# Kernel optimization log

Hardware: AMD Instinct MI355X
Metric: run time of the kernel (lower is better)

## Reference

```python
import jax, jax.numpy as jnp
import numpy as np

PC_RANGE = np.array([-40.0, -40.0, -1.0, 40.0, 40.0, 5.4], np.float32)
RADIUS = 39.0
STEP_SIZE = 0.5
WORLD_LEN = 200
NUM_CLASSES = 17
FAST_THRES = 1e-7
W_ENT = 0.01
W_DIST = 0.01
W_SEM = 1.0
ALPHA_INIT = 1e-6

_xyz_min_w = PC_RANGE[:3]
_xyz_max_w = PC_RANGE[3:]
_rng = _xyz_max_w - _xyz_min_w
BG_LEN = float((np.floor_divide(_rng[0], 2.0) - RADIUS) / RADIUS)
SCENE_CENTER = ((_xyz_min_w + _xyz_max_w) * 0.5).astype(np.float32)
_Z = float(_rng[2] / _rng[0])
XYZ_MIN = np.array([-1.0 - BG_LEN, -1.0 - BG_LEN, -_Z], np.float32)
XYZ_MAX = np.array([1.0 + BG_LEN, 1.0 + BG_LEN, _Z], np.float32)
ACT_SHIFT = float(np.log(1.0 / (1.0 - ALPHA_INIT) - 1.0))
DIST_THRES = (2.0 + 2.0 * BG_LEN) / WORLD_LEN * STEP_SIZE * 0.95

N_INNER = int(2.0 / (2.0 + 2.0 * BG_LEN) * WORLD_LEN / STEP_SIZE) + 1
N_OUTER = N_INNER // 15
_b_in = np.linspace(0.0, 2.0, N_INNER + 1)
_b_out = 2.0 / np.linspace(1.0, 1.0 / 64.0, N_OUTER + 1)
T_VALS = np.concatenate([(_b_in[1:] + _b_in[:-1]) * 0.5, (_b_out[1:] + _b_out[:-1]) * 0.5]).astype(np.float32)

_freq = np.array([1163161, 2309034, 188743, 2997643, 20317180, 852476, 243808, 2457947, 497017, 2731022, 7224789, 214411435, 5565043, 63191967, 76098082, 128860031, 141625221], np.float64)
CLASS_W = (1.0 / np.log(_freq + 0.001)).astype(np.float32)


def trilinear(vol, g):
    # vol: [X,Y,Z,C]; g: [P,3] fractional voxel indices (align_corners=True, zeros padding)
    sizes = jnp.array(vol.shape[:3])
    g0f = jnp.floor(g)
    frac = g - g0f
    g0 = g0f.astype(jnp.int32)
    out = jnp.zeros((g.shape[0], vol.shape[3]), vol.dtype)
    for dx in (0, 1):
        for dy in (0, 1):
            for dz in (0, 1):
                off = jnp.array([dx, dy, dz])
                idx = g0 + off
                w = jnp.prod(jnp.where(off == 1, frac, 1.0 - frac), axis=-1)
                valid = jnp.all((idx >= 0) & (idx < sizes), axis=-1)
                ic = jnp.clip(idx, 0, sizes - 1)
                v = vol[ic[:, 0], ic[:, 1], ic[:, 2]]
                out = out + (w * valid)[:, None] * v
    return out


def _render_losses(density_b, semantic_b, rays_b, bda_b):
    t = jnp.asarray(T_VALS)  # [S]
    gt_depth = rays_b[:, 2]
    gt_depth = jnp.where(gt_depth > 52.0, 0.0, gt_depth)
    ray_valid = gt_depth > 0.0  # [N]
    gt_sem = rays_b[:, 3].astype(jnp.int32)
    ro = rays_b[:, 4:7]
    rd = rays_b[:, 7:10]
    rays_o = (ro - SCENE_CENTER) / RADIUS
    rays_d = rd / jnp.linalg.norm(rd, axis=-1, keepdims=True)
    pts = rays_o[:, None, :] + rays_d[:, None, :] * t[None, :, None]  # [N,S,3]
    nrm = jnp.linalg.norm(pts, axis=-1, keepdims=True)
    inner = (nrm <= 1.0)[..., 0]
    pts = jnp.where(nrm <= 1.0, pts, pts / nrm * (1.0 + BG_LEN - BG_LEN / nrm))
    pts = jnp.einsum('ij,nsj->nsi', bda_b, pts)
    # cumdist_thres: sequential cumulative-distance scan per ray (keep outer points spaced > thres)
    dist = jnp.linalg.norm(pts[:, 1:] - pts[:, :-1], axis=-1)  # [N,S-1]
    def step(cum, d):
        cum = cum + d
        over = cum > DIST_THRES
        return jnp.where(over, 0.0, cum), over
    _, over = jax.lax.scan(step, jnp.zeros(pts.shape[0], pts.dtype), dist.T)
    keep = jnp.concatenate([inner[:, :1], inner[:, 1:] | over.T], axis=1)
    # trilinear grid sample (align_corners=True)
    g = (pts - XYZ_MIN) / (XYZ_MAX - XYZ_MIN)
    gi = (g * (jnp.array([200.0, 200.0, 16.0]) - 1.0)).reshape(-1, 3)
    dens = trilinear(density_b[..., None], gi)[:, 0].reshape(pts.shape[:2])  # [N,S]
    sem = trilinear(semantic_b, gi).reshape(pts.shape[0], pts.shape[1], NUM_CLASSES)  # [N,S,C]
    # Raw2Alpha with interval=0.5: alpha = 1 - (1+exp(d+shift))^(-interval)
    alpha = 1.0 - jnp.power(1.0 + jnp.exp(dens + ACT_SHIFT), -0.5)
    alpha = jnp.where(keep & ray_valid[:, None], alpha, 0.0)
    alpha = jnp.where(alpha > FAST_THRES, alpha, 0.0)  # fast_color_thres cull
    # Alphas2Weights: per-ray exclusive transmittance cumprod
    om = 1.0 - alpha
    Tinc = jnp.cumprod(om, axis=1)
    Texcl = jnp.concatenate([jnp.ones_like(Tinc[:, :1]), Tinc[:, :-1]], axis=1)
    weights = alpha * Texcl
    alphainv_last = Tinc[:, -1]
    pk = weights > FAST_THRES
    w = jnp.where(pk, weights, 0.0)
    # segment_coo semantic render (segment-sum over step dim)
    sem_r = jnp.einsum('ns,nsc->nc', w, sem)
    logp = jax.nn.log_softmax(sem_r, axis=-1)
    nll = -jnp.take_along_axis(logp, gt_sem[:, None], axis=1)[:, 0]
    cw = jnp.asarray(CLASS_W)
    wy = cw[gt_sem] * ray_valid.astype(cw.dtype)
    loss_sem = jnp.sum(wy * nll) / jnp.maximum(jnp.sum(wy), 1e-12)
    # entropy of last transmittance over valid rays
    p = jnp.clip(alphainv_last, 1e-6, 1.0 - 1e-6)
    ent = -(p * jnp.log(p) + (1.0 - p) * jnp.log(1.0 - p))
    nv = jnp.maximum(jnp.sum(ray_valid), 1)
    loss_ent = jnp.sum(jnp.where(ray_valid, ent, 0.0)) / nv
    # flatten_eff_distloss with interval = 1/n_max
    s = 1.0 - 1.0 / (1.0 + t)
    m = jnp.broadcast_to(s[None, :], w.shape)
    n_max = jnp.maximum(jnp.sum(pk), 1)
    interval = 1.0 / n_max
    wm = w * m
    wp = jnp.cumsum(w, axis=1) - w
    wmp = jnp.cumsum(wm, axis=1) - wm
    loss_bi = 2.0 * w * (m * wp - wmp)
    loss_uni = (1.0 / 3.0) * interval * w * w
    loss_dist = (jnp.sum(loss_bi) + jnp.sum(loss_uni)) / nv
    return W_SEM * loss_sem, W_ENT * loss_ent, W_DIST * loss_dist


def setup_inputs():
    key = jax.random.key(0)
    ks = jax.random.split(key, 6)
    B, N = 1, 8192
    density = jax.random.normal(ks[0], (B, 200, 200, 16), jnp.float32)
    semantic = jax.random.normal(ks[1], (B, 200, 200, 16, 17), jnp.float32)
    depth = jax.random.uniform(ks[2], (B, N), jnp.float32, 0.1, 60.0)
    sem_lbl = jax.random.randint(ks[3], (B, N), 0, 17).astype(jnp.float32)
    ro = jax.random.normal(ks[4], (B, N, 3), jnp.float32) + jnp.array([0.0, 0.0, 1.5])
    rd = jax.random.normal(ks[5], (B, N, 3), jnp.float32)
    rd = rd / jnp.linalg.norm(rd, axis=-1, keepdims=True)
    rays = jnp.concatenate([jnp.zeros((B, N, 2)), depth[..., None], sem_lbl[..., None], ro, rd], axis=-1)
    bda = jnp.broadcast_to(jnp.eye(3, dtype=jnp.float32), (B, 3, 3))
    return {"density": density, "semantic": semantic, "rays": rays, "bda": bda}


def reference(density, semantic, rays, bda):
    B = density.shape[0]
    ls, le, ld = 0.0, 0.0, 0.0
    for b in range(B):
        a, c, d = _render_losses(density[b], semantic[b], rays[b], bda[b])
        ls, le, ld = ls + a, le + c, ld + d
    return (ls / B, le / B, ld / B)
```

## Files before the change

### kernel.cpp

```cpp
#include <hip/hip_runtime.h>
#include <math.h>


#define DXX 200
#define DYY 200
#define DZZ 16
#define NC 17
#define S_TOT 416
#define N_IN 390
#define CHUNKS 7
#define RPB 4

typedef float v4u __attribute__((ext_vector_type(4), aligned(4), may_alias));

__constant__ double c_freq[NC] = {1163161.0, 2309034.0, 188743.0, 2997643.0,
  20317180.0, 852476.0, 243808.0, 2457947.0, 497017.0, 2731022.0, 7224789.0,
  214411435.0, 5565043.0, 63191967.0, 76098082.0, 128860031.0, 141625221.0};

__device__ __forceinline__ float iscan_add(float x, int lane) {
#pragma unroll
  for (int off = 1; off < 64; off <<= 1) {
    float y = __shfl_up(x, off);
    if (lane >= off) x += y;
  }
  return x;
}
__device__ __forceinline__ float iscan_mul(float x, int lane) {
#pragma unroll
  for (int off = 1; off < 64; off <<= 1) {
    float y = __shfl_up(x, off);
    if (lane >= off) x *= y;
  }
  return x;
}

__global__ __launch_bounds__(256) void nerf_zero(float* acc) {
  if (threadIdx.x < 16) acc[threadIdx.x] = 0.f;
}

__global__ __launch_bounds__(256) void nerf_main(
    const float* __restrict__ density,
    const float* __restrict__ semantic,
    const float* __restrict__ rays,
    const float* __restrict__ bda,
    float* __restrict__ acc_g,
    int nrays) {
  __shared__ float s_t[CHUNKS * 64];
  __shared__ float s_dist[RPB][S_TOT];
  __shared__ unsigned long long s_keep[RPB][CHUNKS];
  __shared__ float s_acc[8];

  const int lane = threadIdx.x & 63;
  const int wv = threadIdx.x >> 6;
  const int ray = blockIdx.x * RPB + wv;

  const double BG = (double)(1.0f / 39.0f);
  const float BGf = (float)BG;
  const float DTH = (float)((2.0 + 2.0 * BG) / 200.0 * 0.5 * 0.95);
  const float xminf = (float)(-1.0 - BG);
  const float xmaxf = (float)(1.0 + BG);
  const float zf = 6.4f / 80.0f;
  const float sxy = 199.0f / (xmaxf - xminf);
  const float szc = 15.0f / (zf + zf);
  const float ACTS = -13.815509557964274f;

  if (threadIdx.x < 8) s_acc[threadIdx.x] = 0.f;

  for (int i = threadIdx.x; i < CHUNKS * 64; i += 256) {
    double td;
    if (i < N_IN) {
      td = (2.0 * i + 1.0) / 390.0;
    } else {
      int j = i - N_IN;
      const double stp = (1.0 / 64.0 - 1.0) / 26.0;
      double l0 = 1.0 + j * stp;
      double l1 = (j + 1 >= 26) ? (1.0 / 64.0) : (1.0 + (j + 1) * stp);
      td = 1.0 / l0 + 1.0 / l1;
    }
    s_t[i] = (float)td;
  }
  __syncthreads();

  bool doit = false;
  float rox = 0, roy = 0, roz = 0, rdx = 0, rdy = 0, rdz = 0;
  float b00 = 0, b01 = 0, b02 = 0, b10 = 0, b11 = 0, b12 = 0, b20 = 0, b21 = 0, b22 = 0;
  int ysem = 0;
  if (ray < nrays) {
    const float* rp = rays + (size_t)ray * 10;
    float dep = rp[2];
    doit = (dep > 0.f) && (dep <= 52.f);
    ysem = (int)rp[3];
    ysem = ysem < 0 ? 0 : (ysem > NC - 1 ? NC - 1 : ysem);
    const float czc = (-1.0f + 5.4f) * 0.5f;
    rox = rp[4] / 39.0f;
    roy = rp[5] / 39.0f;
    roz = (rp[6] - czc) / 39.0f;
    float d0 = rp[7], d1 = rp[8], d2 = rp[9];
    float rn = sqrtf(d0 * d0 + d1 * d1 + d2 * d2);
    rdx = d0 / rn; rdy = d1 / rn; rdz = d2 / rn;
    b00 = bda[0]; b01 = bda[1]; b02 = bda[2];
    b10 = bda[3]; b11 = bda[4]; b12 = bda[5];
    b20 = bda[6]; b21 = bda[7]; b22 = bda[8];
  }

  auto compute_pt = [&](int s, float& tx, float& ty, float& tz, float& tt,
                        bool& inner) {
    tt = s_t[s];
    float qx = rox + rdx * tt;
    float qy = roy + rdy * tt;
    float qz = roz + rdz * tt;
    float nr = sqrtf(qx * qx + qy * qy + qz * qz);
    inner = (nr <= 1.0f) && (s < S_TOT);
    if (nr > 1.0f) {
      float sc = (1.0f + BGf - BGf / nr) / nr;
      qx *= sc; qy *= sc; qz *= sc;
    }
    tx = b00 * qx + b01 * qy + b02 * qz;
    ty = b10 * qx + b11 * qy + b12 * qz;
    tz = b20 * qx + b21 * qy + b22 * qz;
  };

  if (doit) {
    for (int c = 0; c < CHUNKS; c++) {
      int s = c * 64 + lane;
      float tx, ty, tz, tt; bool inner;
      compute_pt(s, tx, ty, tz, tt, inner);
      unsigned long long bal = __ballot(inner);
      if (lane == 0) s_keep[wv][c] = bal;
      float nx = __shfl(tx, lane + 1);
      float ny = __shfl(ty, lane + 1);
      float nz = __shfl(tz, lane + 1);
      if (c < CHUNKS - 1) {
        float hx, hy, hz, ht; bool hi;
        compute_pt((c + 1) * 64, hx, hy, hz, ht, hi);
        if (lane == 63) { nx = hx; ny = hy; nz = hz; }
      }
      if (s < S_TOT - 1) {
        float ex = nx - tx, ey = ny - ty, ez = nz - tz;
        s_dist[wv][s] = sqrtf(ex * ex + ey * ey + ez * ez);
      }
    }
  }
  __syncthreads();

  if (doit && lane == 0) {
    float cum = 0.f;
    for (int c = 0; c < CHUNKS; c++) {
      unsigned long long k = s_keep[wv][c];
      int b0 = (c == 0) ? 1 : 0;
      for (int b = b0; b < 64; b++) {
        int s = c * 64 + b;
        if (s >= S_TOT) break;
        cum += s_dist[wv][s - 1];
        if (cum > DTH) { cum = 0.f; k |= (1ull << b); }
      }
      s_keep[wv][c] = k;
    }
  }
  __syncthreads();

  float out_sem[NC];
  if (doit) {
#pragma unroll
    for (int j = 0; j < NC; j++) out_sem[j] = 0.f;
    float carry = 1.f, carryW = 0.f, carryWM = 0.f;
    float sum_bi = 0.f, sum_w2 = 0.f, pkcf = 0.f;

    for (int c = 0; c < CHUNKS; c++) {
      int s = c * 64 + lane;
      float tx, ty, tz, tt; bool inner;
      compute_pt(s, tx, ty, tz, tt, inner);
      float m_ = 1.0f - 1.0f / (1.0f + tt);
      bool keep = (s_keep[wv][c] >> lane) & 1ull;

      int ix = 0, iy = 0, iz = 0;
      float fx = 0.f, fy = 0.f, fz = 0.f;
      float a = 0.f;
      if (keep) {
        float gx = (tx - xminf) * sxy;
        float gy = (ty - xminf) * sxy;
        float gz = (tz + zf) * szc;
        float hx = floorf(gx), hy = floorf(gy), hz = floorf(gz);
        ix = (int)hx; iy = (int)hy; iz = (int)hz;
        fx = gx - hx; fy = gy - hy; fz = gz - hz;
        float wx0 = 1.f - fx, wy0 = 1.f - fy, wz0 = 1.f - fz;
        bool vx0 = (unsigned)ix < (unsigned)DXX, vx1 = (unsigned)(ix + 1) < (unsigned)DXX;
        bool vy0 = (unsigned)iy < (unsigned)DYY, vy1 = (unsigned)(iy + 1) < (unsigned)DYY;
        bool vz0 = (unsigned)iz < (unsigned)DZZ, vz1 = (unsigned)(iz + 1) < (unsigned)DZZ;
        float dens = 0.f;
        if (vx0 && vy0 && vz0) dens += wx0 * wy0 * wz0 * density[((size_t)ix * DYY + iy) * DZZ + iz];
        if (vx0 && vy0 && vz1) dens += wx0 * wy0 * fz  * density[((size_t)ix * DYY + iy) * DZZ + iz + 1];
        if (vx0 && vy1 && vz0) dens += wx0 * fy  * wz0 * density[((size_t)ix * DYY + (iy + 1)) * DZZ + iz];
        if (vx0 && vy1 && vz1) dens += wx0 * fy  * fz  * density[((size_t)ix * DYY + (iy + 1)) * DZZ + iz + 1];
        if (vx1 && vy0 && vz0) dens += fx  * wy0 * wz0 * density[((size_t)(ix + 1) * DYY + iy) * DZZ + iz];
        if (vx1 && vy0 && vz1) dens += fx  * wy0 * fz  * density[((size_t)(ix + 1) * DYY + iy) * DZZ + iz + 1];
        if (vx1 && vy1 && vz0) dens += fx  * fy  * wz0 * density[((size_t)(ix + 1) * DYY + (iy + 1)) * DZZ + iz];
        if (vx1 && vy1 && vz1) dens += fx  * fy  * fz  * density[((size_t)(ix + 1) * DYY + (iy + 1)) * DZZ + iz + 1];
        float u = expf(dens + ACTS);
        a = -expm1f(-0.5f * log1pf(u));
        if (!(a > 1e-7f)) a = 0.f;
      }

      float om = 1.f - a;
      float ip = iscan_mul(om, lane);
      float ex = __shfl_up(ip, 1); if (lane == 0) ex = 1.f;
      float wgt = a * carry * ex;
      carry *= __shfl(ip, 63);
      float w = (wgt > 1e-7f) ? wgt : 0.f;
      if (w > 0.f) pkcf += 1.f;

      float wm = w * m_;
      float isw = iscan_add(w, lane);
      float iswm = iscan_add(wm, lane);
      float exw = __shfl_up(isw, 1);  if (lane == 0) exw = 0.f;
      float exwm = __shfl_up(iswm, 1); if (lane == 0) exwm = 0.f;
      sum_bi += 2.f * w * (m_ * (carryW + exw) - (carryWM + exwm));
      sum_w2 += w * w;
      carryW += __shfl(isw, 63);
      carryWM += __shfl(iswm, 63);

      if (w > 0.f) {
        float wx0 = 1.f - fx, wy0 = 1.f - fy, wz0 = 1.f - fz;
        bool vx0 = (unsigned)ix < (unsigned)DXX, vx1 = (unsigned)(ix + 1) < (unsigned)DXX;
        bool vy0 = (unsigned)iy < (unsigned)DYY, vy1 = (unsigned)(iy + 1) < (unsigned)DYY;
        bool vz0 = (unsigned)iz < (unsigned)DZZ, vz1 = (unsigned)(iz + 1) < (unsigned)DZZ;
#define SEM_CORNER(V, WX, WY, WZ, XI, YI, ZI)                                      \
        if (V) {                                                                    \
          float wc = w * (WX) * (WY) * (WZ);                                        \
          const float* sp = semantic + (((size_t)(XI) * DYY + (YI)) * DZZ + (ZI)) * NC; \
          const v4u* sp4 = (const v4u*)sp;                                          \
          v4u q0 = sp4[0], q1 = sp4[1], q2 = sp4[2], q3 = sp4[3];                   \
          float qs = sp[16];                                                        \
          out_sem[0]  += wc * q0[0];  out_sem[1]  += wc * q0[1];                    \
          out_sem[2]  += wc * q0[2];  out_sem[3]  += wc * q0[3];                    \
          out_sem[4]  += wc * q1[0];  out_sem[5]  += wc * q1[1];                    \
          out_sem[6]  += wc * q1[2];  out_sem[7]  += wc * q1[3];                    \
          out_sem[8]  += wc * q2[0];  out_sem[9]  += wc * q2[1];                    \
          out_sem[10] += wc * q2[2];  out_sem[11] += wc * q2[3];                    \
          out_sem[12] += wc * q3[0];  out_sem[13] += wc * q3[1];                    \
          out_sem[14] += wc * q3[2];  out_sem[15] += wc * q3[3];                    \
          out_sem[16] += wc * qs;                                                   \
        }
        SEM_CORNER(vx0 && vy0 && vz0, wx0, wy0, wz0, ix, iy, iz)
        SEM_CORNER(vx0 && vy0 && vz1, wx0, wy0, fz,  ix, iy, iz + 1)
        SEM_CORNER(vx0 && vy1 && vz0, wx0, fy,  wz0, ix, iy + 1, iz)
        SEM_CORNER(vx0 && vy1 && vz1, wx0, fy,  fz,  ix, iy + 1, iz + 1)
        SEM_CORNER(vx1 && vy0 && vz0, fx,  wy0, wz0, ix + 1, iy, iz)
        SEM_CORNER(vx1 && vy0 && vz1, fx,  wy0, fz,  ix + 1, iy, iz + 1)
        SEM_CORNER(vx1 && vy1 && vz0, fx,  fy,  wz0, ix + 1, iy + 1, iz)
        SEM_CORNER(vx1 && vy1 && vz1, fx,  fy,  fz,  ix + 1, iy + 1, iz + 1)
#undef SEM_CORNER
      }
    }

    float r0 = sum_bi, r1 = sum_w2, r2 = pkcf;
#pragma unroll
    for (int off = 32; off >= 1; off >>= 1) {
      r0 += __shfl_xor(r0, off);
      r1 += __shfl_xor(r1, off);
      r2 += __shfl_xor(r2, off);
#pragma unroll
      for (int j = 0; j < NC; j++) out_sem[j] += __shfl_xor(out_sem[j], off);
    }
    if (lane == 0) {
      float M = out_sem[0];
#pragma unroll
      for (int j = 1; j < NC; j++) M = fmaxf(M, out_sem[j]);
      float se = 0.f;
#pragma unroll
      for (int j = 0; j < NC; j++) se += expf(out_sem[j] - M);
      float lse = M + logf(se);
      float sy = 0.f;
#pragma unroll
      for (int j = 0; j < NC; j++) if (j == ysem) sy = out_sem[j];
      float nll = lse - sy;
      float cw = (float)(1.0 / log(c_freq[ysem] + 0.001));
      float p = fminf(fmaxf(carry, 1e-6f), 1.0f - 1e-6f);
      float ent = -(p * logf(p) + (1.f - p) * logf(1.f - p));
      atomicAdd(&s_acc[0], cw * nll);
      atomicAdd(&s_acc[1], cw);
      atomicAdd(&s_acc[2], ent);
      atomicAdd(&s_acc[3], 1.f);
      atomicAdd(&s_acc[4], r0);
      atomicAdd(&s_acc[5], r1);
      atomicAdd(&s_acc[6], r2);
    }
  }

  __syncthreads();
  if (threadIdx.x == 0 && s_acc[3] > 0.f) {
#pragma unroll
    for (int i = 0; i < 7; i++) atomicAdd(&acc_g[i], s_acc[i]);
  }
}

__global__ __launch_bounds__(64) void nerf_fin(const float* __restrict__ acc,
                                               float* __restrict__ out) {
  if (threadIdx.x == 0) {
    float ls = acc[0] / fmaxf(acc[1], 1e-12f);
    float nv = fmaxf(acc[3], 1.f);
    float le = acc[2] / nv;
    float nmax = fmaxf(acc[6], 1.f);
    float ld = (acc[4] + (1.f / 3.f) * (1.f / nmax) * acc[5]) / nv;
    out[0] = 1.0f * ls;
    out[1] = 0.01f * le;
    out[2] = 0.01f * ld;
  }
}

extern "C" void kernel_launch(void* const* d_in, const int* in_sizes, int n_in,
                              void* d_out, int out_size, void* d_ws, size_t ws_size,
                              hipStream_t stream) {
  const float* density = (const float*)d_in[0];
  const float* semantic = (const float*)d_in[1];
  const float* rays = (const float*)d_in[2];
  const float* bda = (const float*)d_in[3];
  float* out = (float*)d_out;
  float* acc = (float*)d_ws;
  int nrays = in_sizes[2] / 10;
  nerf_zero<<<1, 256, 0, stream>>>(acc);
  int nb = (nrays + RPB - 1) / RPB;
  nerf_main<<<nb, 64 * RPB, 0, stream>>>(density, semantic, rays, bda, acc, nrays);
  nerf_fin<<<1, 64, 0, stream>>>(acc, out);
}
```

Baseline: 305.3 us.

## Use persistent waves with atomic ray queue and fuse sample passes

Replaces one-ray-per-wave launch with a capped persistent grid in which each wave pulls rays from an atomic counter, skipping invalid rays immediately. Merges the density sampling into the first pass, skipping gathers for chunks whose z is fully out of the grid, and keeps alpha in registers. Replaces the serial distance filter with a bitmask and ffs walk that only visits short segments. Adds vector loads for fully interior corners. It relies on the counter in the workspace being zeroed and on wave-local LDS ordering replacing block barriers, and it costs more registers.

```diff
diff --git a/kernel.cpp b/kernel.cpp
--- a/kernel.cpp
+++ b/kernel.cpp
@@ -10,8 +10,10 @@
 #define N_IN 390
 #define CHUNKS 7
 #define RPB 4
+#define NBLOCKS 1280
 
 typedef float v4u __attribute__((ext_vector_type(4), aligned(4), may_alias));
+typedef float v2u __attribute__((ext_vector_type(2), aligned(4), may_alias));
 
 __constant__ double c_freq[NC] = {1163161.0, 2309034.0, 188743.0, 2997643.0,
   20317180.0, 852476.0, 243808.0, 2457947.0, 497017.0, 2731022.0, 7224789.0,
@@ -38,7 +40,7 @@
   if (threadIdx.x < 16) acc[threadIdx.x] = 0.f;
 }
 
-__global__ __launch_bounds__(256) void nerf_main(
+__global__ __launch_bounds__(256, 5) void nerf_main(
     const float* __restrict__ density,
     const float* __restrict__ semantic,
     const float* __restrict__ rays,
@@ -48,19 +50,18 @@
   __shared__ float s_t[CHUNKS * 64];
   __shared__ float s_dist[RPB][S_TOT];
   __shared__ unsigned long long s_keep[RPB][CHUNKS];
+  __shared__ unsigned long long s_big[RPB][CHUNKS];
   __shared__ float s_acc[8];
 
   const int lane = threadIdx.x & 63;
   const int wv = threadIdx.x >> 6;
-  const int ray = blockIdx.x * RPB + wv;
 
   const double BG = (double)(1.0f / 39.0f);
   const float BGf = (float)BG;
   const float DTH = (float)((2.0 + 2.0 * BG) / 200.0 * 0.5 * 0.95);
   const float xminf = (float)(-1.0 - BG);
-  const float xmaxf = (float)(1.0 + BG);
   const float zf = 6.4f / 80.0f;
-  const float sxy = 199.0f / (xmaxf - xminf);
+  const float sxy = 199.0f / ((float)(1.0 + BG) - xminf);
   const float szc = 15.0f / (zf + zf);
   const float ACTS = -13.815509557964274f;
 
@@ -81,52 +82,59 @@
   }
   __syncthreads();
 
-  bool doit = false;
-  float rox = 0, roy = 0, roz = 0, rdx = 0, rdy = 0, rdz = 0;
-  float b00 = 0, b01 = 0, b02 = 0, b10 = 0, b11 = 0, b12 = 0, b20 = 0, b21 = 0, b22 = 0;
-  int ysem = 0;
-  if (ray < nrays) {
+  const float A0 = -expm1f(-0.5f * log1pf(expf(ACTS)));
+
+  const float b00 = bda[0], b01 = bda[1], b02 = bda[2];
+  const float b10 = bda[3], b11 = bda[4], b12 = bda[5];
+  const float b20 = bda[6], b21 = bda[7], b22 = bda[8];
+
+  int* cnt = (int*)(acc_g + 8);
+
+  for (;;) {
+    int ray;
+    if (lane == 0) ray = atomicAdd(cnt, 1);
+    ray = __shfl(ray, 0);
+    if (ray >= nrays) break;
+
     const float* rp = rays + (size_t)ray * 10;
     float dep = rp[2];
-    doit = (dep > 0.f) && (dep <= 52.f);
-    ysem = (int)rp[3];
+    bool doit = (dep > 0.f) && (dep <= 52.f);
+    if (!doit) continue;
+    int ysem = (int)rp[3];
     ysem = ysem < 0 ? 0 : (ysem > NC - 1 ? NC - 1 : ysem);
     const float czc = (-1.0f + 5.4f) * 0.5f;
-    rox = rp[4] / 39.0f;
-    roy = rp[5] / 39.0f;
-    roz = (rp[6] - czc) / 39.0f;
+    float rox = rp[4] / 39.0f;
+    float roy = rp[5] / 39.0f;
+    float roz = (rp[6] - czc) / 39.0f;
     float d0 = rp[7], d1 = rp[8], d2 = rp[9];
     float rn = sqrtf(d0 * d0 + d1 * d1 + d2 * d2);
-    rdx = d0 / rn; rdy = d1 / rn; rdz = d2 / rn;
-    b00 = bda[0]; b01 = bda[1]; b02 = bda[2];
-    b10 = bda[3]; b11 = bda[4]; b12 = bda[5];
-    b20 = bda[6]; b21 = bda[7]; b22 = bda[8];
-  }
-
-  auto compute_pt = [&](int s, float& tx, float& ty, float& tz, float& tt,
-                        bool& inner) {
-    tt = s_t[s];
-    float qx = rox + rdx * tt;
-    float qy = roy + rdy * tt;
-    float qz = roz + rdz * tt;
-    float nr = sqrtf(qx * qx + qy * qy + qz * qz);
-    inner = (nr <= 1.0f) && (s < S_TOT);
-    if (nr > 1.0f) {
-      float sc = (1.0f + BGf - BGf / nr) / nr;
-      qx *= sc; qy *= sc; qz *= sc;
-    }
-    tx = b00 * qx + b01 * qy + b02 * qz;
-    ty = b10 * qx + b11 * qy + b12 * qz;
-    tz = b20 * qx + b21 * qy + b22 * qz;
-  };
-
-  if (doit) {
+    float rdx = d0 / rn, rdy = d1 / rn, rdz = d2 / rn;
+
+    auto compute_pt = [&](int s, float& tx, float& ty, float& tz, float& tt,
+                          bool& inner) {
+      tt = s_t[s];
+      float qx = rox + rdx * tt;
+      float qy = roy + rdy * tt;
+      float qz = roz + rdz * tt;
+      float nr = sqrtf(qx * qx + qy * qy + qz * qz);
+      inner = (nr <= 1.0f) && (s < S_TOT);
+      if (nr > 1.0f) {
+        float sc = (1.0f + BGf - BGf / nr) / nr;
+        qx *= sc; qy *= sc; qz *= sc;
+      }
+      tx = b00 * qx + b01 * qy + b02 * qz;
+      ty = b10 * qx + b11 * qy + b12 * qz;
+      tz = b20 * qx + b21 * qy + b22 * qz;
+    };
+
+    float a_r[CHUNKS];
+    int hotmask = 0;
+#pragma unroll
     for (int c = 0; c < CHUNKS; c++) {
       int s = c * 64 + lane;
       float tx, ty, tz, tt; bool inner;
       compute_pt(s, tx, ty, tz, tt, inner);
       unsigned long long bal = __ballot(inner);
-      if (lane == 0) s_keep[wv][c] = bal;
       float nx = __shfl(tx, lane + 1);
       float ny = __shfl(ty, lane + 1);
       float nz = __shfl(tz, lane + 1);
@@ -135,71 +143,113 @@
         compute_pt((c + 1) * 64, hx, hy, hz, ht, hi);
         if (lane == 63) { nx = hx; ny = hy; nz = hz; }
       }
-      if (s < S_TOT - 1) {
-        float ex = nx - tx, ey = ny - ty, ez = nz - tz;
-        s_dist[wv][s] = sqrtf(ex * ex + ey * ey + ez * ez);
-      }
-    }
-  }
-  __syncthreads();
-
-  if (doit && lane == 0) {
-    float cum = 0.f;
-    for (int c = 0; c < CHUNKS; c++) {
-      unsigned long long k = s_keep[wv][c];
-      int b0 = (c == 0) ? 1 : 0;
-      for (int b = b0; b < 64; b++) {
-        int s = c * 64 + b;
-        if (s >= S_TOT) break;
-        cum += s_dist[wv][s - 1];
-        if (cum > DTH) { cum = 0.f; k |= (1ull << b); }
-      }
-      s_keep[wv][c] = k;
-    }
-  }
-  __syncthreads();
-
-  float out_sem[NC];
-  if (doit) {
-#pragma unroll
-    for (int j = 0; j < NC; j++) out_sem[j] = 0.f;
-    float carry = 1.f, carryW = 0.f, carryWM = 0.f;
-    float sum_bi = 0.f, sum_w2 = 0.f, pkcf = 0.f;
-
-    for (int c = 0; c < CHUNKS; c++) {
-      int s = c * 64 + lane;
-      float tx, ty, tz, tt; bool inner;
-      compute_pt(s, tx, ty, tz, tt, inner);
-      float m_ = 1.0f - 1.0f / (1.0f + tt);
-      bool keep = (s_keep[wv][c] >> lane) & 1ull;
-
-      int ix = 0, iy = 0, iz = 0;
-      float fx = 0.f, fy = 0.f, fz = 0.f;
-      float a = 0.f;
-      if (keep) {
+      float ex = nx - tx, ey = ny - ty, ez = nz - tz;
+      float dd = sqrtf(ex * ex + ey * ey + ez * ez);
+      bool dlive = (s < S_TOT - 1);
+      if (dlive) s_dist[wv][s] = dd;
+      unsigned long long db = __ballot(dlive && (dd > DTH));
+      if (lane == 0) { s_keep[wv][c] = bal; s_big[wv][c] = db; }
+
+      bool live = s < S_TOT;
+      float gz = (tz + zf) * szc;
+      float hzf = floorf(gz);
+      int iz = (int)hzf;
+      float fz = gz - hzf;
+      bool vz0 = (unsigned)iz < (unsigned)DZZ;
+      bool vz1 = (unsigned)(iz + 1) < (unsigned)DZZ;
+      bool zv = live && (vz0 || vz1);
+      float a;
+      if (__any(zv)) {
+        hotmask |= (1 << c);
         float gx = (tx - xminf) * sxy;
         float gy = (ty - xminf) * sxy;
-        float gz = (tz + zf) * szc;
-        float hx = floorf(gx), hy = floorf(gy), hz = floorf(gz);
-        ix = (int)hx; iy = (int)hy; iz = (int)hz;
-        fx = gx - hx; fy = gy - hy; fz = gz - hz;
+        float hxf = floorf(gx), hyf = floorf(gy);
+        int ix = (int)hxf, iy = (int)hyf;
+        float fx = gx - hxf, fy = gy - hyf;
         float wx0 = 1.f - fx, wy0 = 1.f - fy, wz0 = 1.f - fz;
         bool vx0 = (unsigned)ix < (unsigned)DXX, vx1 = (unsigned)(ix + 1) < (unsigned)DXX;
         bool vy0 = (unsigned)iy < (unsigned)DYY, vy1 = (unsigned)(iy + 1) < (unsigned)DYY;
-        bool vz0 = (unsigned)iz < (unsigned)DZZ, vz1 = (unsigned)(iz + 1) < (unsigned)DZZ;
         float dens = 0.f;
-        if (vx0 && vy0 && vz0) dens += wx0 * wy0 * wz0 * density[((size_t)ix * DYY + iy) * DZZ + iz];
-        if (vx0 && vy0 && vz1) dens += wx0 * wy0 * fz  * density[((size_t)ix * DYY + iy) * DZZ + iz + 1];
-        if (vx0 && vy1 && vz0) dens += wx0 * fy  * wz0 * density[((size_t)ix * DYY + (iy + 1)) * DZZ + iz];
-        if (vx0 && vy1 && vz1) dens += wx0 * fy  * fz  * density[((size_t)ix * DYY + (iy + 1)) * DZZ + iz + 1];
-        if (vx1 && vy0 && vz0) dens += fx  * wy0 * wz0 * density[((size_t)(ix + 1) * DYY + iy) * DZZ + iz];
-        if (vx1 && vy0 && vz1) dens += fx  * wy0 * fz  * density[((size_t)(ix + 1) * DYY + iy) * DZZ + iz + 1];
-        if (vx1 && vy1 && vz0) dens += fx  * fy  * wz0 * density[((size_t)(ix + 1) * DYY + (iy + 1)) * DZZ + iz];
-        if (vx1 && vy1 && vz1) dens += fx  * fy  * fz  * density[((size_t)(ix + 1) * DYY + (iy + 1)) * DZZ + iz + 1];
+        if (zv) {
+          int base = (ix * DYY + iy) * DZZ + iz;
+          const float* p0 = density + base;
+          if (vx0 && vx1 && vy0 && vy1 && vz0 && vz1) {
+            v2u d00 = *(const v2u*)(p0);
+            v2u d01 = *(const v2u*)(p0 + DZZ);
+            v2u d10 = *(const v2u*)(p0 + DYY * DZZ);
+            v2u d11 = *(const v2u*)(p0 + DYY * DZZ + DZZ);
+            dens += wx0 * wy0 * wz0 * d00[0];
+            dens += wx0 * wy0 * fz  * d00[1];
+            dens += wx0 * fy  * wz0 * d01[0];
+            dens += wx0 * fy  * fz  * d01[1];
+            dens += fx  * wy0 * wz0 * d10[0];
+            dens += fx  * wy0 * fz  * d10[1];
+            dens += fx  * fy  * wz0 * d11[0];
+            dens += fx  * fy  * fz  * d11[1];
+          } else {
+            if (vx0 && vy0 && vz0) dens += wx0 * wy0 * wz0 * p0[0];
+            if (vx0 && vy0 && vz1) dens += wx0 * wy0 * fz  * p0[1];
+            if (vx0 && vy1 && vz0) dens += wx0 * fy  * wz0 * p0[DZZ];
+            if (vx0 && vy1 && vz1) dens += wx0 * fy  * fz  * p0[DZZ + 1];
+            if (vx1 && vy0 && vz0) dens += fx  * wy0 * wz0 * p0[DYY * DZZ];
+            if (vx1 && vy0 && vz1) dens += fx  * wy0 * fz  * p0[DYY * DZZ + 1];
+            if (vx1 && vy1 && vz0) dens += fx  * fy  * wz0 * p0[DYY * DZZ + DZZ];
+            if (vx1 && vy1 && vz1) dens += fx  * fy  * fz  * p0[DYY * DZZ + DZZ + 1];
+          }
+        }
         float u = expf(dens + ACTS);
         a = -expm1f(-0.5f * log1pf(u));
-        if (!(a > 1e-7f)) a = 0.f;
+      } else {
+        a = A0;
       }
+      a_r[c] = a;
+    }
+
+    asm volatile("s_waitcnt lgkmcnt(0)" ::: "memory");
+    if (lane == 0) {
+      float cum = 0.f;
+      int prev = 0;
+      unsigned long long carrybit = 0;
+#pragma unroll
+      for (int c = 0; c < CHUNKS; c++) {
+        unsigned long long inner = s_keep[wv][c];
+        unsigned long long db = s_big[wv][c];
+        unsigned long long big = (db << 1) | carrybit;
+        carrybit = db >> 63;
+        unsigned long long valid = ~0ull;
+        if (c == 0) valid &= ~1ull;
+        if (c == CHUNKS - 1) valid &= 0x00000000FFFFFFFFull;
+        big &= valid;
+        unsigned long long k = inner | big;
+        unsigned long long nb = valid & ~big;
+        while (nb) {
+          int b = __ffsll((unsigned long long)nb) - 1;
+          nb &= nb - 1;
+          int s = c * 64 + b;
+          if (s - 1 != prev) cum = 0.f;
+          cum += s_dist[wv][s - 1];
+          if (cum > DTH) { cum = 0.f; k |= 1ull << b; }
+          prev = s;
+        }
+        s_keep[wv][c] = k;
+      }
+    }
+    asm volatile("s_waitcnt lgkmcnt(0)" ::: "memory");
+
+    float out_sem[NC];
+#pragma unroll
+    for (int j = 0; j < NC; j++) out_sem[j] = 0.f;
+    float w_r[CHUNKS];
+    float carry = 1.f, carryW = 0.f, carryWM = 0.f;
+    float sum_bi = 0.f, sum_w2 = 0.f, pkcf = 0.f;
+#pragma unroll
+    for (int c = 0; c < CHUNKS; c++) {
+      int s = c * 64 + lane;
+      float tt = s_t[s];
+      float m_ = 1.0f - 1.0f / (1.0f + tt);
+      bool keep = (s_keep[wv][c] >> lane) & 1ull;
+      float ar = a_r[c];
+      float a = (keep && (ar > 1e-7f)) ? ar : 0.f;
 
       float om = 1.f - a;
       float ip = iscan_mul(om, lane);
@@ -218,38 +268,65 @@
       sum_w2 += w * w;
       carryW += __shfl(isw, 63);
       carryWM += __shfl(iswm, 63);
-
+      w_r[c] = w;
+    }
+
+#pragma unroll
+    for (int c = 0; c < CHUNKS; c++) {
+      if (!((hotmask >> c) & 1)) continue;
+      if (!__any(w_r[c] > 0.f)) continue;
+      int s = c * 64 + lane;
+      float tx, ty, tz, tt; bool inner;
+      compute_pt(s, tx, ty, tz, tt, inner);
+      float w = w_r[c];
       if (w > 0.f) {
+        float gx = (tx - xminf) * sxy;
+        float gy = (ty - xminf) * sxy;
+        float gz = (tz + zf) * szc;
+        float hxf = floorf(gx), hyf = floorf(gy), hzf = floorf(gz);
+        int ix = (int)hxf, iy = (int)hyf, iz = (int)hzf;
+        float fx = gx - hxf, fy = gy - hyf, fz = gz - hzf;
         float wx0 = 1.f - fx, wy0 = 1.f - fy, wz0 = 1.f - fz;
         bool vx0 = (unsigned)ix < (unsigned)DXX, vx1 = (unsigned)(ix + 1) < (unsigned)DXX;
         bool vy0 = (unsigned)iy < (unsigned)DYY, vy1 = (unsigned)(iy + 1) < (unsigned)DYY;
         bool vz0 = (unsigned)iz < (unsigned)DZZ, vz1 = (unsigned)(iz + 1) < (unsigned)DZZ;
-#define SEM_CORNER(V, WX, WY, WZ, XI, YI, ZI)                                      \
-        if (V) {                                                                    \
-          float wc = w * (WX) * (WY) * (WZ);                                        \
-          const float* sp = semantic + (((size_t)(XI) * DYY + (YI)) * DZZ + (ZI)) * NC; \
-          const v4u* sp4 = (const v4u*)sp;                                          \
-          v4u q0 = sp4[0], q1 = sp4[1], q2 = sp4[2], q3 = sp4[3];                   \
-          float qs = sp[16];                                                        \
-          out_sem[0]  += wc * q0[0];  out_sem[1]  += wc * q0[1];                    \
-          out_sem[2]  += wc * q0[2];  out_sem[3]  += wc * q0[3];                    \
-          out_sem[4]  += wc * q1[0];  out_sem[5]  += wc * q1[1];                    \
-          out_sem[6]  += wc * q1[2];  out_sem[7]  += wc * q1[3];                    \
-          out_sem[8]  += wc * q2[0];  out_sem[9]  += wc * q2[1];                    \
-          out_sem[10] += wc * q2[2];  out_sem[11] += wc * q2[3];                    \
-          out_sem[12] += wc * q3[0];  out_sem[13] += wc * q3[1];                    \
-          out_sem[14] += wc * q3[2];  out_sem[15] += wc * q3[3];                    \
-          out_sem[16] += wc * qs;                                                   \
+        int base17 = ((ix * DYY + iy) * DZZ + iz) * NC;
+        const float* sp0 = semantic + base17;
+        const float* sp1 = sp0 + DYY * DZZ * NC;
+#define SEM_ACC(PTR, WC)                                                        \
+        { float wc = (WC);                                                      \
+          const v4u* q = (const v4u*)(PTR);                                     \
+          v4u q0 = q[0], q1 = q[1], q2 = q[2], q3 = q[3];                       \
+          float qs = (PTR)[16];                                                 \
+          out_sem[0]  += wc * q0[0];  out_sem[1]  += wc * q0[1];                \
+          out_sem[2]  += wc * q0[2];  out_sem[3]  += wc * q0[3];                \
+          out_sem[4]  += wc * q1[0];  out_sem[5]  += wc * q1[1];                \
+          out_sem[6]  += wc * q1[2];  out_sem[7]  += wc * q1[3];                \
+          out_sem[8]  += wc * q2[0];  out_sem[9]  += wc * q2[1];                \
+          out_sem[10] += wc * q2[2];  out_sem[11] += wc * q2[3];                \
+          out_sem[12] += wc * q3[0];  out_sem[13] += wc * q3[1];                \
+          out_sem[14] += wc * q3[2];  out_sem[15] += wc * q3[3];                \
+          out_sem[16] += wc * qs; }
+        if (vx0 && vx1 && vy0 && vy1 && vz0 && vz1) {
+          SEM_ACC(sp0,                 w * wx0 * wy0 * wz0)
+          SEM_ACC(sp0 + NC,            w * wx0 * wy0 * fz)
+          SEM_ACC(sp0 + DZZ * NC,      w * wx0 * fy  * wz0)
+          SEM_ACC(sp0 + DZZ * NC + NC, w * wx0 * fy  * fz)
+          SEM_ACC(sp1,                 w * fx  * wy0 * wz0)
+          SEM_ACC(sp1 + NC,            w * fx  * wy0 * fz)
+          SEM_ACC(sp1 + DZZ * NC,      w * fx  * fy  * wz0)
+          SEM_ACC(sp1 + DZZ * NC + NC, w * fx  * fy  * fz)
+        } else {
+          if (vx0 && vy0 && vz0) SEM_ACC(sp0,                 w * wx0 * wy0 * wz0)
+          if (vx0 && vy0 && vz1) SEM_ACC(sp0 + NC,            w * wx0 * wy0 * fz)
+          if (vx0 && vy1 && vz0) SEM_ACC(sp0 + DZZ * NC,      w * wx0 * fy  * wz0)
+          if (vx0 && vy1 && vz1) SEM_ACC(sp0 + DZZ * NC + NC, w * wx0 * fy  * fz)
+          if (vx1 && vy0 && vz0) SEM_ACC(sp1,                 w * fx  * wy0 * wz0)
+          if (vx1 && vy0 && vz1) SEM_ACC(sp1 + NC,            w * fx  * wy0 * fz)
+          if (vx1 && vy1 && vz0) SEM_ACC(sp1 + DZZ * NC,      w * fx  * fy  * wz0)
+          if (vx1 && vy1 && vz1) SEM_ACC(sp1 + DZZ * NC + NC, w * fx  * fy  * fz)
         }
-        SEM_CORNER(vx0 && vy0 && vz0, wx0, wy0, wz0, ix, iy, iz)
-        SEM_CORNER(vx0 && vy0 && vz1, wx0, wy0, fz,  ix, iy, iz + 1)
-        SEM_CORNER(vx0 && vy1 && vz0, wx0, fy,  wz0, ix, iy + 1, iz)
-        SEM_CORNER(vx0 && vy1 && vz1, wx0, fy,  fz,  ix, iy + 1, iz + 1)
-        SEM_CORNER(vx1 && vy0 && vz0, fx,  wy0, wz0, ix + 1, iy, iz)
-        SEM_CORNER(vx1 && vy0 && vz1, fx,  wy0, fz,  ix + 1, iy, iz + 1)
-        SEM_CORNER(vx1 && vy1 && vz0, fx,  fy,  wz0, ix + 1, iy + 1, iz)
-        SEM_CORNER(vx1 && vy1 && vz1, fx,  fy,  fz,  ix + 1, iy + 1, iz + 1)
-#undef SEM_CORNER
+#undef SEM_ACC
       }
     }
 
@@ -320,6 +397,7 @@
   int nrays = in_sizes[2] / 10;
   nerf_zero<<<1, 256, 0, stream>>>(acc);
   int nb = (nrays + RPB - 1) / RPB;
+  if (nb > NBLOCKS) nb = NBLOCKS;
   nerf_main<<<nb, 64 * RPB, 0, stream>>>(density, semantic, rays, bda, acc, nrays);
   nerf_fin<<<1, 64, 0, stream>>>(acc, out);
 }
```

Result: slower. 427.3 us (+40.0%).

## Skip serial cum-distance scan via ballot masks, skip empty chunks, fuse finalize

Applied to the files above, without the earlier changes.

A per-chunk ballot now marks samples whose single step distance already exceeds the threshold. The serial lane-0 keep-mask scan then visits only the remaining bits and resets its accumulator across gaps. Chunks with an empty keep mask are skipped in the main render loop. The zero and finalize kernels are replaced by a memset and a last-block-done counter inside the main kernel, removing launches at the cost of an extra global atomic per block and a fence.

```diff
diff --git a/kernel.cpp b/kernel.cpp
--- a/kernel.cpp
+++ b/kernel.cpp
@@ -10,8 +10,10 @@
 #define N_IN 390
 #define CHUNKS 7
 #define RPB 4
+#define CNT_OFF 128
 
 typedef float v4u __attribute__((ext_vector_type(4), aligned(4), may_alias));
+typedef float v2u __attribute__((ext_vector_type(2), aligned(4), may_alias));
 
 __constant__ double c_freq[NC] = {1163161.0, 2309034.0, 188743.0, 2997643.0,
   20317180.0, 852476.0, 243808.0, 2457947.0, 497017.0, 2731022.0, 7224789.0,
@@ -32,10 +34,6 @@
     if (lane >= off) x *= y;
   }
   return x;
-}
-
-__global__ __launch_bounds__(256) void nerf_zero(float* acc) {
-  if (threadIdx.x < 16) acc[threadIdx.x] = 0.f;
 }
 
 __global__ __launch_bounds__(256) void nerf_main(
@@ -44,10 +42,12 @@
     const float* __restrict__ rays,
     const float* __restrict__ bda,
     float* __restrict__ acc_g,
+    float* __restrict__ out,
     int nrays) {
   __shared__ float s_t[CHUNKS * 64];
   __shared__ float s_dist[RPB][S_TOT];
   __shared__ unsigned long long s_keep[RPB][CHUNKS];
+  __shared__ unsigned long long s_big[RPB][CHUNKS];
   __shared__ float s_acc[8];
 
   const int lane = threadIdx.x & 63;
@@ -58,9 +58,8 @@
   const float BGf = (float)BG;
   const float DTH = (float)((2.0 + 2.0 * BG) / 200.0 * 0.5 * 0.95);
   const float xminf = (float)(-1.0 - BG);
-  const float xmaxf = (float)(1.0 + BG);
   const float zf = 6.4f / 80.0f;
-  const float sxy = 199.0f / (xmaxf - xminf);
+  const float sxy = 199.0f / ((float)(1.0 + BG) - xminf);
   const float szc = 15.0f / (zf + zf);
   const float ACTS = -13.815509557964274f;
 
@@ -126,7 +125,6 @@
       float tx, ty, tz, tt; bool inner;
       compute_pt(s, tx, ty, tz, tt, inner);
       unsigned long long bal = __ballot(inner);
-      if (lane == 0) s_keep[wv][c] = bal;
       float nx = __shfl(tx, lane + 1);
       float ny = __shfl(ty, lane + 1);
       float nz = __shfl(tz, lane + 1);
@@ -135,43 +133,61 @@
         compute_pt((c + 1) * 64, hx, hy, hz, ht, hi);
         if (lane == 63) { nx = hx; ny = hy; nz = hz; }
       }
-      if (s < S_TOT - 1) {
-        float ex = nx - tx, ey = ny - ty, ez = nz - tz;
-        s_dist[wv][s] = sqrtf(ex * ex + ey * ey + ez * ez);
-      }
+      float ex = nx - tx, ey = ny - ty, ez = nz - tz;
+      float dd = sqrtf(ex * ex + ey * ey + ez * ez);
+      bool dlive = (s < S_TOT - 1);
+      if (dlive) s_dist[wv][s] = dd;
+      unsigned long long db = __ballot(dlive && (dd > DTH));
+      if (lane == 0) { s_keep[wv][c] = bal; s_big[wv][c] = db; }
     }
   }
   __syncthreads();
 
   if (doit && lane == 0) {
     float cum = 0.f;
+    int prev = 0;
+    unsigned long long carrybit = 0;
+#pragma unroll
     for (int c = 0; c < CHUNKS; c++) {
-      unsigned long long k = s_keep[wv][c];
-      int b0 = (c == 0) ? 1 : 0;
-      for (int b = b0; b < 64; b++) {
+      unsigned long long inner = s_keep[wv][c];
+      unsigned long long db = s_big[wv][c];
+      unsigned long long big = (db << 1) | carrybit;
+      carrybit = db >> 63;
+      unsigned long long vmask = ~0ull;
+      if (c == 0) vmask &= ~1ull;
+      if (c == CHUNKS - 1) vmask &= 0x00000000FFFFFFFFull;
+      big &= vmask;
+      unsigned long long k = inner | big;
+      unsigned long long nb = vmask & ~big;
+      while (nb) {
+        int b = __ffsll((unsigned long long)nb) - 1;
+        nb &= nb - 1;
         int s = c * 64 + b;
-        if (s >= S_TOT) break;
+        if (s - 1 != prev) cum = 0.f;
         cum += s_dist[wv][s - 1];
-        if (cum > DTH) { cum = 0.f; k |= (1ull << b); }
+        if (cum > DTH) { cum = 0.f; k |= 1ull << b; }
+        prev = s;
       }
       s_keep[wv][c] = k;
     }
   }
   __syncthreads();
 
-  float out_sem[NC];
   if (doit) {
+    float out_sem[NC];
 #pragma unroll
     for (int j = 0; j < NC; j++) out_sem[j] = 0.f;
     float carry = 1.f, carryW = 0.f, carryWM = 0.f;
     float sum_bi = 0.f, sum_w2 = 0.f, pkcf = 0.f;
 
     for (int c = 0; c < CHUNKS; c++) {
+      unsigned long long km = s_keep[wv][c];
+      if (km == 0ull) continue;
       int s = c * 64 + lane;
       float tx, ty, tz, tt; bool inner;
       compute_pt(s, tx, ty, tz, tt, inner);
       float m_ = 1.0f - 1.0f / (1.0f + tt);
-      bool keep = (s_keep[wv][c] >> lane) & 1ull;
+      bool keep = (km >> lane) & 1ull;
 
       int ix = 0, iy = 0, iz = 0;
       float fx = 0.f, fy = 0.f, fz = 0.f;
@@ -288,23 +304,26 @@
   }
 
   __syncthreads();
-  if (threadIdx.x == 0 && s_acc[3] > 0.f) {
-#pragma unroll
-    for (int i = 0; i < 7; i++) atomicAdd(&acc_g[i], s_acc[i]);
-  }
-}
-
-__global__ __launch_bounds__(64) void nerf_fin(const float* __restrict__ acc,
-                                               float* __restrict__ out) {
   if (threadIdx.x == 0) {
-    float ls = acc[0] / fmaxf(acc[1], 1e-12f);
-    float nv = fmaxf(acc[3], 1.f);
-    float le = acc[2] / nv;
-    float nmax = fmaxf(acc[6], 1.f);
-    float ld = (acc[4] + (1.f / 3.f) * (1.f / nmax) * acc[5]) / nv;
-    out[0] = 1.0f * ls;
-    out[1] = 0.01f * le;
-    out[2] = 0.01f * ld;
+    if (s_acc[3] > 0.f) {
+#pragma unroll
+      for (int i = 0; i < 7; i++) atomicAdd(&acc_g[i], s_acc[i]);
+    }
+    asm volatile("s_waitcnt vmcnt(0)" ::: "memory");
+    int prev = atomicAdd((int*)acc_g + CNT_OFF, 1);
+    if (prev == (int)gridDim.x - 1) {
+      float t[7];
+#pragma unroll
+      for (int j = 0; j < 7; j++) t[j] = atomicAdd(&acc_g[j], 0.f);
+      float ls = t[0] / fmaxf(t[1], 1e-12f);
+      float nv = fmaxf(t[3], 1.f);
+      float le = t[2] / nv;
+      float nmax = fmaxf(t[6], 1.f);
+      float ld = (t[4] + (1.f / 3.f) * (1.f / nmax) * t[5]) / nv;
+      out[0] = 1.0f * ls;
+      out[1] = 0.01f * le;
+      out[2] = 0.01f * ld;
+    }
   }
 }
 
@@ -318,8 +337,8 @@
   float* out = (float*)d_out;
   float* acc = (float*)d_ws;
   int nrays = in_sizes[2] / 10;
-  nerf_zero<<<1, 256, 0, stream>>>(acc);
   int nb = (nrays + RPB - 1) / RPB;
-  nerf_main<<<nb, 64 * RPB, 0, stream>>>(density, semantic, rays, bda, acc, nrays);
-  nerf_fin<<<1, 64, 0, stream>>>(acc, out);
+  hipMemsetAsync(d_ws, 0, 516, stream);
+  nerf_main<<<nb, 64 * RPB, 0, stream>>>(density, semantic, rays, bda, acc, out,
+                                         nrays);
 }
```

After: 323.1 us. +5.8%, slower.
